# Optimization experiments

Measured on AMD Instinct MI355X. Metric: run time of the kernel, lower is better.

Reference implementation:

```python
import jax, jax.numpy as jnp
import numpy as np

N_NODES = 100000
NEG_SLOPE = 0.2


def setup_inputs() -> dict:
    key = jax.random.key(0)
    k1, k2, k3, k4, k5 = jax.random.split(key, 5)
    N, E, Fin, Fout = N_NODES, 3200000, 128, 128
    x = jax.random.normal(k1, (N, Fin), dtype=jnp.float32)
    edge_index = jax.random.randint(k2, (2, E), 0, N, dtype=jnp.int64)
    # xavier-uniform for lin weight (fan_in=Fin, fan_out=Fout)
    limit = float(np.sqrt(6.0 / (Fin + Fout)))
    W = jax.random.uniform(k3, (Fin, Fout), jnp.float32, -limit, limit)
    # PyG glorot init for attention vectors (fan ~ Fout)
    alim = float(np.sqrt(6.0 / (1 + Fout)))
    att_src = jax.random.uniform(k4, (Fout,), jnp.float32, -alim, alim)
    att_dst = jax.random.uniform(k5, (Fout,), jnp.float32, -alim, alim)
    bias = jnp.zeros((Fout,), jnp.float32)
    return {"x": x, "edge_index": edge_index, "W": W,
            "att_src": att_src, "att_dst": att_dst, "bias": bias}


def reference(x, edge_index, W, att_src, att_dst, bias):
    N = x.shape[0]
    src, dst = edge_index[0], edge_index[1]  # messages flow src -> dst
    h = x @ W                                # [N, Fout]
    a_src = h @ att_src                      # [N]
    a_dst = h @ att_dst                      # [N]
    e = a_src[src] + a_dst[dst]              # [E]
    e = jax.nn.leaky_relu(e, NEG_SLOPE)
    # segment softmax over incoming edges of each dst node
    e_max = jax.ops.segment_max(e, dst, num_segments=N)  # [N]
    e_max = jnp.where(jnp.isfinite(e_max), e_max, 0.0)
    e_exp = jnp.exp(e - e_max[dst])          # [E]
    denom = jax.ops.segment_sum(e_exp, dst, num_segments=N)  # [N]
    alpha = e_exp / (denom[dst] + 1e-16)     # [E]
    # scatter-add weighted neighbor features
    out = jax.ops.segment_sum(alpha[:, None] * h[src], dst, num_segments=N)
    out = out + bias
    return jax.nn.relu(out)
```

## Files before the change

### kernel.cpp

```cpp
#include <hip/hip_runtime.h>
#include <cstdint>
#include <cstddef>

#define NEG 0.2f
#define CAP 10752
#define FINE_CAP CAP

typedef __attribute__((ext_vector_type(8))) short short8;
typedef __attribute__((ext_vector_type(4))) float f32x4;

__device__ __forceinline__ unsigned short f2bf(float f) {
  unsigned u = __float_as_uint(f);
  unsigned r = (u + 0x7fffu + ((u >> 16) & 1u)) >> 16;
  return (unsigned short)r;
}

__global__ __launch_bounds__(512) void k_detect(const int* __restrict__ ei32,
                                                int* __restrict__ flag,
                                                int* __restrict__ cursor,
                                                const float* __restrict__ W,
                                                unsigned short* __restrict__ Wt) {
  int t = threadIdx.x;
  cursor[t] = t * CAP;
  if (t < 64) {
    int v = ei32[2 * t + 1];
    unsigned long long b = __ballot(v != 0);
    if (t == 0) flag[0] = (b == 0ULL) ? 1 : 0;
  }
#pragma unroll
  for (int i = 0; i < 8; ++i) {
    int idx = i * 512 + t;
    float4 v = ((const float4*)W)[idx];
    int k = idx >> 5;
    int c = (idx & 31) * 4;
    Wt[(c + 0) * 128 + k] = f2bf(v.x);
    Wt[(c + 1) * 128 + k] = f2bf(v.y);
    Wt[(c + 2) * 128 + k] = f2bf(v.z);
    Wt[(c + 3) * 128 + k] = f2bf(v.w);
  }
}

__device__ __forceinline__ int edge_val(const void* ei, long long idx, int is64) {
  return is64 ? (int)((const long long*)ei)[idx] : ((const int*)ei)[idx];
}

#define MS_CHUNK 4096
__global__ __launch_bounds__(256) void k_fused(
    const float* __restrict__ x, const unsigned short* __restrict__ Wt,
    const float* __restrict__ as_, const float* __restrict__ ad_,
    unsigned short* __restrict__ hb, float* __restrict__ a_s,
    float* __restrict__ a_d, int N,
    const void* __restrict__ ei, const int* __restrict__ flag,
    int* __restrict__ cursor, uint32_t* __restrict__ buck, int E, int nms) {
  __shared__ int hist[512];
  __shared__ int resv[512];
  int gid = blockIdx.x;
  int t = threadIdx.x;
  bool is_ms = ((gid % 3) == 0) && ((gid / 3) < nms);

  if (is_ms) {
    int bid = gid / 3;
    const int is64 = flag[0];
    for (int i = t; i < 512; i += 256) hist[i] = 0;
    __syncthreads();
    long long base = (long long)bid * MS_CHUNK;
    uint32_t rec[16];
    int bb[16], rk[16];
#pragma unroll
    for (int i = 0; i < 16; ++i) {
      long long idx = base + i * 256 + t;
      bb[i] = -1;
      if (idx < E) {
        int s = edge_val(ei, idx, is64);
        int d = edge_val(ei, (long long)E + idx, is64);
        bb[i] = d >> 8;
        rec[i] = ((uint32_t)(d & 255) << 17) | (uint32_t)s;
        rk[i] = atomicAdd(&hist[bb[i]], 1);
      }
    }
    __syncthreads();
    for (int b = t; b < 512; b += 256) {
      int c = hist[b];
      resv[b] = c ? atomicAdd(&cursor[b], c) : 0;
    }
    __syncthreads();
#pragma unroll
    for (int i = 0; i < 16; ++i) {
      if (bb[i] >= 0) buck[(size_t)resv[bb[i]] + rk[i]] = rec[i];
    }
    return;
  }

  int gemm_id = gid - min(gid / 3 + 1, nms);
  int lane = t & 63;
  int wv = t >> 6;
  int row0 = gemm_id * 64 + wv * 16;
  int r = lane & 15, o = lane >> 4;

  int arow = row0 + r;
  if (arow >= N) arow = N - 1;
  const float* xr = x + (size_t)arow * 128 + o * 8;
  short8 a[4];
#pragma unroll
  for (int kt = 0; kt < 4; ++kt) {
    float4 lo = *(const float4*)(xr + kt * 32);
    float4 hi = *(const float4*)(xr + kt * 32 + 4);
    short8 av;
    av[0] = (short)f2bf(lo.x); av[1] = (short)f2bf(lo.y);
    av[2] = (short)f2bf(lo.z); av[3] = (short)f2bf(lo.w);
    av[4] = (short)f2bf(hi.x); av[5] = (short)f2bf(hi.y);
    av[6] = (short)f2bf(hi.z); av[7] = (short)f2bf(hi.w);
    a[kt] = av;
  }

  float ats[8], atd[8];
#pragma unroll
  for (int ct = 0; ct < 8; ++ct) {
    ats[ct] = as_[ct * 16 + r];
    atd[ct] = ad_[ct * 16 + r];
  }

  f32x4 acc[8];
#pragma unroll
  for (int ct = 0; ct < 8; ++ct) acc[ct] = (f32x4){0.f, 0.f, 0.f, 0.f};
#pragma unroll
  for (int ct = 0; ct < 8; ++ct) {
    const unsigned short* wb = Wt + ((size_t)(ct * 16 + r)) * 128 + o * 8;
#pragma unroll
    for (int kt = 0; kt < 4; ++kt) {
      short8 b = *(const short8*)(wb + kt * 32);
      acc[ct] = __builtin_amdgcn_mfma_f32_16x16x32_bf16(a[kt], b, acc[ct], 0, 0, 0);
    }
  }

#pragma unroll
  for (int j = 0; j < 4; ++j) {
    int row = row0 + o * 4 + j;
    bool ok = row < N;
    float ps = 0.f, pd = 0.f;
#pragma unroll
    for (int ct = 0; ct < 8; ++ct) {
      float v = acc[ct][j];
      if (ok) hb[(size_t)row * 128 + ct * 16 + r] = f2bf(v);
      ps += v * ats[ct];
      pd += v * atd[ct];
    }
#pragma unroll
    for (int d = 1; d <= 8; d <<= 1) {
      ps += __shfl_xor(ps, d);
      pd += __shfl_xor(pd, d);
    }
    if (ok && r == 0) { a_s[row] = ps; a_d[row] = pd; }
  }
}

__global__ __launch_bounds__(512) void k_bscan(const int* __restrict__ cursor,
                                               int* __restrict__ base,
                                               int NB, int E) {
  __shared__ int wsum[8];
  int t = threadIdx.x;
  int v = (t < NB) ? (cursor[t] - t * CAP) : 0;
  int lane = t & 63, w = t >> 6;
  int incl = v;
#pragma unroll
  for (int d = 1; d < 64; d <<= 1) {
    int o = __shfl_up(incl, d);
    if (lane >= d) incl += o;
  }
  if (lane == 63) wsum[w] = incl;
  __syncthreads();
  int woff = 0;
  for (int i = 0; i < w; ++i) woff += wsum[i];
  int excl = woff + incl - v;
  if (t < NB) base[t] = excl;
  if (t == 0) base[NB] = E;
}

__global__ __launch_bounds__(1024) void k_fine(const int* __restrict__ base,
                                               const int* __restrict__ cursor,
                                               const uint32_t* __restrict__ buck,
                                               const float* __restrict__ a_s,
                                               const float* __restrict__ a_d,
                                               int* __restrict__ offsets,
                                               int2* __restrict__ sw,
                                               int N, int E) {
  __shared__ int hist[256];
  __shared__ int cur[256];
  __shared__ int wsum[4];
  __shared__ float ad_sh[256];
  __shared__ uint32_t stage[FINE_CAP];
  int b = blockIdx.x;
  int t = threadIdx.x;
  int b0 = base[b];
  int cnt = cursor[b] - b * CAP;
  const uint32_t* bk = buck + (size_t)b * CAP;
  int node = (b << 8) + (t & 255);
  if (t < 256) {
    hist[t] = 0;
    ad_sh[t] = (node < N) ? a_d[node] : 0.f;
  }
  __syncthreads();
  for (int i = t; i < cnt; i += 1024) atomicAdd(&hist[bk[i] >> 17], 1);
  __syncthreads();
  int v = 0, incl = 0;
  int lane = t & 63, w4 = t >> 6;
  if (t < 256) {
    v = hist[t];
    incl = v;
#pragma unroll
    for (int d = 1; d < 64; d <<= 1) {
      int o = __shfl_up(incl, d);
      if (lane >= d) incl += o;
    }
    if (lane == 63) wsum[w4] = incl;
  }
  __syncthreads();
  if (t < 256) {
    int woff = 0;
    for (int i = 0; i < w4; ++i) woff += wsum[i];
    int excl = woff + incl - v;
    cur[t] = excl;
    if (node < N) offsets[node] = b0 + excl;
  }
  if (b == 0 && t == 0) offsets[N] = E;
  __syncthreads();
  for (int i = t; i < cnt; i += 1024) {
    uint32_t r = bk[i];
    int pos = atomicAdd(&cur[r >> 17], 1);
    stage[pos] = r;
  }
  __syncthreads();
  for (int i = t; i < cnt; i += 1024) {
    uint32_t r = stage[i];
    int s = (int)(r & 0x1ffffu);
    float e = a_s[s] + ad_sh[r >> 17];
    e = (e > 0.f) ? e : NEG * e;
    sw[b0 + i] = make_int2(s, __float_as_int(__expf(e)));
  }
}

#define AGG_LOAD(K, JJ)                                                   \
  {                                                                       \
    int e_ = ((JJ) * 4 + g) & 63;                                         \
    int ss_ = __shfl(s_l, e_);                                            \
    float ww_ = __shfl(w_l, e_);                                          \
    w##K = ((JJ) < iters) ? ww_ : 0.f;                                    \
    u##K = *(const uint4*)&hb[(size_t)ss_ * 128 + l16 * 8];               \
  }

#define AGG_FMA(K)                                                        \
  {                                                                       \
    acc[0] += w##K * __uint_as_float(u##K.x << 16);                       \
    acc[1] += w##K * __uint_as_float(u##K.x & 0xffff0000u);               \
    acc[2] += w##K * __uint_as_float(u##K.y << 16);                       \
    acc[3] += w##K * __uint_as_float(u##K.y & 0xffff0000u);               \
    acc[4] += w##K * __uint_as_float(u##K.z << 16);                       \
    acc[5] += w##K * __uint_as_float(u##K.z & 0xffff0000u);               \
    acc[6] += w##K * __uint_as_float(u##K.w << 16);                       \
    acc[7] += w##K * __uint_as_float(u##K.w & 0xffff0000u);               \
  }

__global__ __launch_bounds__(256) void k_agg(const int* __restrict__ offs,
                                             const int2* __restrict__ sw,
                                             const unsigned short* __restrict__ hb,
                                             const float* __restrict__ bias,
                                             float* __restrict__ out, int N) {
  int lane = threadIdx.x & 63;
  int n = blockIdx.x * 4 + (threadIdx.x >> 6);
  if (n >= N) return;
  int g = lane >> 4;
  int l16 = lane & 15;
  float acc[8] = {};
  float sum = 0.f;
  int s0 = offs[n], s1 = offs[n + 1];

  for (int base = s0; base < s1; base += 64) {
    int idx = base + lane;
    int s_l = 0;
    float w_l = 0.f;
    if (idx < s1) {
      int2 m = sw[idx];
      s_l = m.x;
      w_l = __int_as_float(m.y);
    }
    sum += w_l;
    int cnt = min(64, s1 - base);
    int iters = (cnt + 3) >> 2;
    uint4 u0, u1, u2, u3, u4;
    float w0, w1, w2, w3, w4;
    AGG_LOAD(0, 0) AGG_LOAD(1, 1) AGG_LOAD(2, 2)
    AGG_LOAD(3, 3) AGG_LOAD(4, 4)
    int j = 0;
    for (; j + 5 < iters; j += 5) {
      AGG_FMA(0) AGG_LOAD(0, j + 5)
      AGG_FMA(1) AGG_LOAD(1, j + 6)
      AGG_FMA(2) AGG_LOAD(2, j + 7)
      AGG_FMA(3) AGG_LOAD(3, j + 8)
      AGG_FMA(4) AGG_LOAD(4, j + 9)
    }
    AGG_FMA(0) AGG_FMA(1) AGG_FMA(2) AGG_FMA(3) AGG_FMA(4)
  }
#pragma unroll
  for (int d = 1; d <= 32; d <<= 1) sum += __shfl_xor(sum, d);
#pragma unroll
  for (int d = 16; d <= 32; d <<= 1) {
#pragma unroll
    for (int i = 0; i < 8; ++i) acc[i] += __shfl_xor(acc[i], d);
  }
  float inv = 1.0f / (sum + 1e-16f);
  if (lane < 32) {
    int half = g & 1;
    int f = l16 * 8 + half * 4;
    float4 bv = *(const float4*)&bias[f];
    float4 o;
    o.x = fmaxf(acc[half * 4 + 0] * inv + bv.x, 0.f);
    o.y = fmaxf(acc[half * 4 + 1] * inv + bv.y, 0.f);
    o.z = fmaxf(acc[half * 4 + 2] * inv + bv.z, 0.f);
    o.w = fmaxf(acc[half * 4 + 3] * inv + bv.w, 0.f);
    *(float4*)&out[(size_t)n * 128 + f] = o;
  }
}

extern "C" void kernel_launch(void* const* d_in, const int* in_sizes, int n_in,
                              void* d_out, int out_size, void* d_ws, size_t ws_size,
                              hipStream_t stream) {
  const float* x = (const float*)d_in[0];
  const void* ei = d_in[1];
  const float* W = (const float*)d_in[2];
  const float* att_s = (const float*)d_in[3];
  const float* att_d = (const float*)d_in[4];
  const float* bias = (const float*)d_in[5];
  float* out = (float*)d_out;

  const int N = in_sizes[0] / 128;
  const int E = in_sizes[1] / 2;
  const int NB = (N + 255) >> 8;

  uint8_t* ws = (uint8_t*)d_ws;
  size_t off = 0;
  auto alloc = [&](size_t bytes) -> void* {
    void* p = ws + off;
    off = (off + bytes + 511) & ~(size_t)511;
    return p;
  };
  int* flag = (int*)alloc(4);
  int* bcur = (int*)alloc(512 * 4);
  int* bbase = (int*)alloc(513 * 4);
  unsigned short* Wt = (unsigned short*)alloc(128 * 128 * 2);
  int* offsets = (int*)alloc((size_t)(N + 1) * 4);
  int2* sw = (int2*)alloc((size_t)E * 8);
  unsigned short* hb = (unsigned short*)alloc((size_t)N * 128 * 2);
  float* a_s = (float*)alloc((size_t)N * 4);
  float* a_d = (float*)alloc((size_t)N * 4);
  uint32_t* buck = (uint32_t*)d_out;
  (void)ws_size; (void)n_in; (void)out_size;

  const int ngemm = (N + 63) / 64;
  const int nms = (E + MS_CHUNK - 1) / MS_CHUNK;
  int grid = ngemm + nms;
  if (grid < 3 * nms - 2) grid = 3 * nms - 2;

  k_detect<<<1, 512, 0, stream>>>((const int*)ei, flag, bcur, W, Wt);
  k_fused<<<grid, 256, 0, stream>>>(x, Wt, att_s, att_d, hb, a_s, a_d, N,
                                    ei, flag, bcur, buck, E, nms);
  k_bscan<<<1, 512, 0, stream>>>(bcur, bbase, NB, E);
  k_fine<<<NB, 1024, 0, stream>>>(bbase, bcur, buck, a_s, a_d, offsets, sw, N, E);
  k_agg<<<(N + 3) / 4, 256, 0, stream>>>(offsets, sw, hb, bias, out, N);
}
```

Measured before the change: 201.9 us.

## Fuse bucket scan into k_fine and restructure aggregation with packed FMA

Drops the separate single-block k_bscan launch: every k_fine block recomputes the 512-entry bucket prefix scan itself and keeps only its own base offset. In k_agg, each 16-lane group now loads its edge metadata (source, weight) straight from global memory instead of broadcasting it with lane shuffles. Those metadata loads are prefetched one stage ahead of the feature gathers, and the pipeline depth goes from 5 to 4. Accumulation uses 2-wide float vectors so the compiler can emit packed FMAs; because every lane now adds each weight, the softmax denominator is rescaled by 1/16 to compensate. The risk is redundant scan work in every block and more global load instructions, which mostly hit the same addresses across 16 lanes.

```diff
diff --git a/kernel.cpp b/kernel.cpp
--- a/kernel.cpp
+++ b/kernel.cpp
@@ -8,6 +8,7 @@
 
 typedef __attribute__((ext_vector_type(8))) short short8;
 typedef __attribute__((ext_vector_type(4))) float f32x4;
+typedef __attribute__((ext_vector_type(2))) float f32x2;
 
 __device__ __forceinline__ unsigned short f2bf(float f) {
   unsigned u = __float_as_uint(f);
@@ -154,30 +155,7 @@
   }
 }
 
-__global__ __launch_bounds__(512) void k_bscan(const int* __restrict__ cursor,
-                                               int* __restrict__ base,
-                                               int NB, int E) {
-  __shared__ int wsum[8];
-  int t = threadIdx.x;
-  int v = (t < NB) ? (cursor[t] - t * CAP) : 0;
-  int lane = t & 63, w = t >> 6;
-  int incl = v;
-#pragma unroll
-  for (int d = 1; d < 64; d <<= 1) {
-    int o = __shfl_up(incl, d);
-    if (lane >= d) incl += o;
-  }
-  if (lane == 63) wsum[w] = incl;
-  __syncthreads();
-  int woff = 0;
-  for (int i = 0; i < w; ++i) woff += wsum[i];
-  int excl = woff + incl - v;
-  if (t < NB) base[t] = excl;
-  if (t == 0) base[NB] = E;
-}
-
-__global__ __launch_bounds__(1024) void k_fine(const int* __restrict__ base,
-                                               const int* __restrict__ cursor,
+__global__ __launch_bounds__(1024) void k_fine(const int* __restrict__ cursor,
                                                const uint32_t* __restrict__ buck,
                                                const float* __restrict__ a_s,
                                                const float* __restrict__ a_d,
@@ -186,24 +164,47 @@
                                                int N, int E) {
   __shared__ int hist[256];
   __shared__ int cur[256];
+  __shared__ int wsum8[8];
   __shared__ int wsum[4];
   __shared__ float ad_sh[256];
+  __shared__ int b0_sh;
   __shared__ uint32_t stage[FINE_CAP];
   int b = blockIdx.x;
   int t = threadIdx.x;
-  int b0 = base[b];
+  int lane = t & 63;
   int cnt = cursor[b] - b * CAP;
   const uint32_t* bk = buck + (size_t)b * CAP;
   int node = (b << 8) + (t & 255);
+
+  int sv = 0, sincl = 0, sw8 = t >> 6;
+  if (t < 512) {
+    sv = cursor[t] - t * CAP;
+    sincl = sv;
+#pragma unroll
+    for (int d = 1; d < 64; d <<= 1) {
+      int o = __shfl_up(sincl, d);
+      if (lane >= d) sincl += o;
+    }
+    if (lane == 63) wsum8[sw8] = sincl;
+  }
   if (t < 256) {
     hist[t] = 0;
     ad_sh[t] = (node < N) ? a_d[node] : 0.f;
   }
   __syncthreads();
+  if (t < 512) {
+    int woff = 0;
+    for (int i = 0; i < sw8; ++i) woff += wsum8[i];
+    int excl = woff + sincl - sv;
+    if (t == b) b0_sh = excl;
+  }
+  __syncthreads();
+  int b0 = b0_sh;
+
   for (int i = t; i < cnt; i += 1024) atomicAdd(&hist[bk[i] >> 17], 1);
   __syncthreads();
   int v = 0, incl = 0;
-  int lane = t & 63, w4 = t >> 6;
+  int w4 = t >> 6;
   if (t < 256) {
     v = hist[t];
     incl = v;
@@ -239,25 +240,36 @@
   }
 }
 
-#define AGG_LOAD(K, JJ)                                                   \
+#define AGG_META(K, JJ)                                                   \
   {                                                                       \
-    int e_ = ((JJ) * 4 + g) & 63;                                         \
-    int ss_ = __shfl(s_l, e_);                                            \
-    float ww_ = __shfl(w_l, e_);                                          \
-    w##K = ((JJ) < iters) ? ww_ : 0.f;                                    \
-    u##K = *(const uint4*)&hb[(size_t)ss_ * 128 + l16 * 8];               \
+    int e_ = (JJ) * 4 + g;                                                \
+    m##K = swp[(e_ < cnt) ? e_ : 0];                                      \
+    if (e_ >= cnt) m##K.y = 0;         \
+  }
+
+#define AGG_GATH(K)                                                       \
+  {                                                                       \
+    w##K = __int_as_float(m##K.y);                                        \
+    sum += w##K;                                                          \
+    u##K = *(const uint4*)&hb[(size_t)(uint32_t)m##K.x * 128 + l16 * 8];  \
   }
 
 #define AGG_FMA(K)                                                        \
   {                                                                       \
-    acc[0] += w##K * __uint_as_float(u##K.x << 16);                       \
-    acc[1] += w##K * __uint_as_float(u##K.x & 0xffff0000u);               \
-    acc[2] += w##K * __uint_as_float(u##K.y << 16);                       \
-    acc[3] += w##K * __uint_as_float(u##K.y & 0xffff0000u);               \
-    acc[4] += w##K * __uint_as_float(u##K.z << 16);                       \
-    acc[5] += w##K * __uint_as_float(u##K.z & 0xffff0000u);               \
-    acc[6] += w##K * __uint_as_float(u##K.w << 16);                       \
-    acc[7] += w##K * __uint_as_float(u##K.w & 0xffff0000u);               \
+    f32x2 ww; ww[0] = w##K; ww[1] = w##K;                                 \
+    f32x2 p;                                                              \
+    p[0] = __uint_as_float(u##K.x << 16);                                 \
+    p[1] = __uint_as_float(u##K.x & 0xffff0000u);                         \
+    acc2[0] += ww * p;                                                    \
+    p[0] = __uint_as_float(u##K.y << 16);                                 \
+    p[1] = __uint_as_float(u##K.y & 0xffff0000u);                         \
+    acc2[1] += ww * p;                                                    \
+    p[0] = __uint_as_float(u##K.z << 16);                                 \
+    p[1] = __uint_as_float(u##K.z & 0xffff0000u);                         \
+    acc2[2] += ww * p;                                                    \
+    p[0] = __uint_as_float(u##K.w << 16);                                 \
+    p[1] = __uint_as_float(u##K.w & 0xffff0000u);                         \
+    acc2[3] += ww * p;                                                    \
   }
 
 __global__ __launch_bounds__(256) void k_agg(const int* __restrict__ offs,
@@ -270,53 +282,54 @@
   if (n >= N) return;
   int g = lane >> 4;
   int l16 = lane & 15;
-  float acc[8] = {};
+  f32x2 acc2[4];
+#pragma unroll
+  for (int i = 0; i < 4; ++i) { acc2[i][0] = 0.f; acc2[i][1] = 0.f; }
   float sum = 0.f;
   int s0 = offs[n], s1 = offs[n + 1];
 
   for (int base = s0; base < s1; base += 64) {
-    int idx = base + lane;
-    int s_l = 0;
-    float w_l = 0.f;
-    if (idx < s1) {
-      int2 m = sw[idx];
-      s_l = m.x;
-      w_l = __int_as_float(m.y);
-    }
-    sum += w_l;
+    const int2* swp = sw + base;
     int cnt = min(64, s1 - base);
     int iters = (cnt + 3) >> 2;
-    uint4 u0, u1, u2, u3, u4;
-    float w0, w1, w2, w3, w4;
-    AGG_LOAD(0, 0) AGG_LOAD(1, 1) AGG_LOAD(2, 2)
-    AGG_LOAD(3, 3) AGG_LOAD(4, 4)
+    int2 m0, m1, m2, m3;
+    uint4 u0, u1, u2, u3;
+    float w0, w1, w2, w3;
+    AGG_META(0, 0) AGG_META(1, 1) AGG_META(2, 2) AGG_META(3, 3)
+    AGG_GATH(0) AGG_META(0, 4)
+    AGG_GATH(1) AGG_META(1, 5)
+    AGG_GATH(2) AGG_META(2, 6)
+    AGG_GATH(3) AGG_META(3, 7)
     int j = 0;
-    for (; j + 5 < iters; j += 5) {
-      AGG_FMA(0) AGG_LOAD(0, j + 5)
-      AGG_FMA(1) AGG_LOAD(1, j + 6)
-      AGG_FMA(2) AGG_LOAD(2, j + 7)
-      AGG_FMA(3) AGG_LOAD(3, j + 8)
-      AGG_FMA(4) AGG_LOAD(4, j + 9)
-    }
-    AGG_FMA(0) AGG_FMA(1) AGG_FMA(2) AGG_FMA(3) AGG_FMA(4)
+    for (; j + 4 < iters; j += 4) {
+      AGG_FMA(0) AGG_GATH(0) AGG_META(0, j + 8)
+      AGG_FMA(1) AGG_GATH(1) AGG_META(1, j + 9)
+      AGG_FMA(2) AGG_GATH(2) AGG_META(2, j + 10)
+      AGG_FMA(3) AGG_GATH(3) AGG_META(3, j + 11)
+    }
+    AGG_FMA(0) AGG_FMA(1) AGG_FMA(2) AGG_FMA(3)
   }
 #pragma unroll
   for (int d = 1; d <= 32; d <<= 1) sum += __shfl_xor(sum, d);
 #pragma unroll
   for (int d = 16; d <= 32; d <<= 1) {
 #pragma unroll
-    for (int i = 0; i < 8; ++i) acc[i] += __shfl_xor(acc[i], d);
-  }
+    for (int i = 0; i < 4; ++i) {
+      acc2[i][0] += __shfl_xor(acc2[i][0], d);
+      acc2[i][1] += __shfl_xor(acc2[i][1], d);
+    }
+  }
+  sum *= 0.0625f;
   float inv = 1.0f / (sum + 1e-16f);
   if (lane < 32) {
     int half = g & 1;
     int f = l16 * 8 + half * 4;
     float4 bv = *(const float4*)&bias[f];
     float4 o;
-    o.x = fmaxf(acc[half * 4 + 0] * inv + bv.x, 0.f);
-    o.y = fmaxf(acc[half * 4 + 1] * inv + bv.y, 0.f);
-    o.z = fmaxf(acc[half * 4 + 2] * inv + bv.z, 0.f);
-    o.w = fmaxf(acc[half * 4 + 3] * inv + bv.w, 0.f);
+    o.x = fmaxf(acc2[half * 2 + 0][0] * inv + bv.x, 0.f);
+    o.y = fmaxf(acc2[half * 2 + 0][1] * inv + bv.y, 0.f);
+    o.z = fmaxf(acc2[half * 2 + 1][0] * inv + bv.z, 0.f);
+    o.w = fmaxf(acc2[half * 2 + 1][1] * inv + bv.w, 0.f);
     *(float4*)&out[(size_t)n * 128 + f] = o;
   }
 }
@@ -345,7 +358,6 @@
   };
   int* flag = (int*)alloc(4);
   int* bcur = (int*)alloc(512 * 4);
-  int* bbase = (int*)alloc(513 * 4);
   unsigned short* Wt = (unsigned short*)alloc(128 * 128 * 2);
   int* offsets = (int*)alloc((size_t)(N + 1) * 4);
   int2* sw = (int2*)alloc((size_t)E * 8);
@@ -363,7 +375,6 @@
   k_detect<<<1, 512, 0, stream>>>((const int*)ei, flag, bcur, W, Wt);
   k_fused<<<grid, 256, 0, stream>>>(x, Wt, att_s, att_d, hb, a_s, a_d, N,
                                     ei, flag, bcur, buck, E, nms);
-  k_bscan<<<1, 512, 0, stream>>>(bcur, bbase, NB, E);
-  k_fine<<<NB, 1024, 0, stream>>>(bbase, bcur, buck, a_s, a_d, offsets, sw, N, E);
+  k_fine<<<NB, 1024, 0, stream>>>(bcur, buck, a_s, a_d, offsets, sw, N, E);
   k_agg<<<(N + 3) / 4, 256, 0, stream>>>(offsets, sw, hb, bias, out, N);
 }
```

New measurement: 219.3 us. +8.6%, slower.
